# Optimization experiments

Measured on AMD Instinct MI355X. Metric: run time of the kernel, lower is better.

Reference implementation:

```python
import jax, jax.numpy as jnp
import numpy as np

N_HEADS = 16


def _apply_rope(x, rope):
    # x: [B, H, N, Dh], rope: [B, N, Dh]; consecutive (even, odd) pairs form complex numbers
    xr, xi = x[..., 0::2], x[..., 1::2]              # [B,H,N,Dh/2]
    rr, ri = rope[:, None, :, 0::2], rope[:, None, :, 1::2]  # [B,1,N,Dh/2]
    or_ = xr * rr - xi * ri
    oi = xr * ri + xi * rr
    return jnp.stack([or_, oi], axis=-1).reshape(x.shape)


def setup_inputs() -> dict:
    key = jax.random.key(0)
    ks = jax.random.split(key, 8)
    B, N, D, Dh = 2, 2048, 2048, 128
    s = 0.02
    return {
        "x": jax.random.normal(ks[0], (B, N, D), jnp.float32),
        "q_rope": jax.random.normal(ks[1], (B, N, Dh), jnp.float32),
        "k_rope": jax.random.normal(ks[2], (B, N, Dh), jnp.float32),
        "Wq": jax.random.normal(ks[3], (D, D), jnp.float32) * s,
        "Wk": jax.random.normal(ks[4], (D, D), jnp.float32) * s,
        "Wv": jax.random.normal(ks[5], (D, D), jnp.float32) * s,
        "Wo": jax.random.normal(ks[6], (D, D), jnp.float32) * s,
        "bo": jax.random.normal(ks[7], (D,), jnp.float32) * s,
    }


def reference(x, q_rope, k_rope, Wq, Wk, Wv, Wo, bo):
    B, N, D = x.shape
    H = N_HEADS
    Dh = D // H
    # QKV projections (weights stored as [in, out])
    q = (x @ Wq).reshape(B, N, H, Dh).transpose(0, 2, 1, 3)  # [B,H,N,Dh]
    k = (x @ Wk).reshape(B, N, H, Dh).transpose(0, 2, 1, 3)
    v = (x @ Wv).reshape(B, N, H, Dh).transpose(0, 2, 1, 3)
    # NOTE: original scales q by d_head^-0.5 AND F.sdpa applies its default
    # 1/sqrt(d_head) scale again -> total score scale 1/d_head (faithful).
    q = q * (Dh ** -0.5)
    q = _apply_rope(q, q_rope)
    k = _apply_rope(k, k_rope)
    scores = jnp.einsum('bhnd,bhmd->bhnm', q, k) * (Dh ** -0.5)
    attn = jax.nn.softmax(scores, axis=-1)
    out = jnp.einsum('bhnm,bhmd->bhnd', attn, v)  # [B,H,N,Dh]
    out = out.transpose(0, 2, 1, 3).reshape(B, N, D)
    return out @ Wo + bo
```

## Files before the change

kernel.cpp:

```cpp
#include <hip/hip_runtime.h>
#include <hip/hip_bf16.h>
#include <stdint.h>


typedef __attribute__((ext_vector_type(4))) float f32x4;
typedef __attribute__((ext_vector_type(8))) short bf16x8;

__device__ __forceinline__ unsigned short f2bf(float f){
  unsigned u = __builtin_bit_cast(unsigned, f);
  u += 0x7FFFu + ((u >> 16) & 1u);
  return (unsigned short)(u >> 16);
}
__device__ __forceinline__ float bf2f(unsigned short h){
  unsigned u = ((unsigned)h) << 16;
  return __builtin_bit_cast(float, u);
}
__device__ __forceinline__ void gload16(const void* g, void* l){
  __builtin_amdgcn_global_load_lds((const __attribute__((address_space(1))) void*)g,
                                   (__attribute__((address_space(3))) void*)l, 16, 0, 0);
}
__device__ __forceinline__ void drain_all(){
  asm volatile("s_waitcnt vmcnt(0) lgkmcnt(0)" ::: "memory");
  __builtin_amdgcn_sched_barrier(0);
}

__global__ void k_prep(const float* __restrict__ W0, const float* __restrict__ W1,
                       const float* __restrict__ W2, const float* __restrict__ W3,
                       unsigned short* __restrict__ WT,
                       const float* __restrict__ x, unsigned short* __restrict__ xb){
  if (blockIdx.z == 4){
    int bid = blockIdx.y * 32 + blockIdx.x;
    int t = threadIdx.x;
    #pragma unroll
    for (int it = 0; it < 8; it++){
      int i = bid * 2048 + it * 256 + t;
      float4 v = ((const float4*)x)[i];
      unsigned long long pk = (unsigned long long)f2bf(v.x)
        | ((unsigned long long)f2bf(v.y) << 16)
        | ((unsigned long long)f2bf(v.z) << 32)
        | ((unsigned long long)f2bf(v.w) << 48);
      ((unsigned long long*)xb)[i] = pk;
    }
    return;
  }
  const float* W = (blockIdx.z == 0) ? W0 : (blockIdx.z == 1) ? W1 : (blockIdx.z == 2) ? W2 : W3;
  unsigned short* dst = WT + (size_t)blockIdx.z * 4194304;
  __shared__ float tile[64][65];
  int t = threadIdx.x;
  int cc = t & 63, rb = t >> 6;
  int bx = blockIdx.x * 64;
  int by = blockIdx.y * 64;
  #pragma unroll
  for (int i = 0; i < 16; i++){
    int r = rb + i * 4;
    tile[r][cc] = W[(size_t)(by + r) * 2048 + bx + cc];
  }
  __syncthreads();
  #pragma unroll
  for (int i = 0; i < 16; i++){
    int r = rb + i * 4;
    dst[(size_t)(bx + r) * 2048 + by + cc] = f2bf(tile[cc][r]);
  }
}

__global__ __launch_bounds__(256, 4) void k_gemm_qkv(
    const unsigned short* __restrict__ A,
    const unsigned short* __restrict__ Bt,
    unsigned short* __restrict__ Oq,
    unsigned short* __restrict__ Ok,
    unsigned short* __restrict__ Ov,
    const float* __restrict__ ropeq,
    const float* __restrict__ ropek)
{
  const int Kdim = 2048;
  __shared__ unsigned short As[128 * 64];
  __shared__ unsigned short Bs[128 * 64];
  const int tid = threadIdx.x;
  const int w = tid >> 6, l = tid & 63, g = l >> 4, c = l & 15;
  const int i0 = blockIdx.y * 32 + blockIdx.x;
  const int xcd = i0 & 7, r0 = i0 >> 3;
  const int bm = (xcd * 4 + (r0 & 3)) * 128;
  const int bn = (r0 >> 2) * 128;
  const int mw = (w >> 1) * 64, nw = (w & 1) * 64;
  f32x4 acc[4][4] = {};
  const int srow = l >> 3;
  const int sbyte = (((l & 7) ^ srow) << 4);
  const char* Ab = (const char*)A;
  const char* Bb = (const char*)Bt;
  char* AsB = (char*)As; char* BsB = (char*)Bs;

  for (int kt = 0; kt < Kdim; kt += 64){
    __syncthreads();
    #pragma unroll
    for (int j = 0; j < 4; j++){
      int chunk = w * 4 + j;
      int row = chunk * 8 + srow;
      gload16(Ab + ((size_t)(bm + row) * Kdim + kt) * 2 + sbyte, AsB + chunk * 1024);
      gload16(Bb + ((size_t)(bn + row) * Kdim + kt) * 2 + sbyte, BsB + chunk * 1024);
    }
    __syncthreads();
    #pragma unroll
    for (int kk = 0; kk < 2; kk++){
      bf16x8 av[4], bv[4];
      #pragma unroll
      for (int i = 0; i < 4; i++){
        int m = mw + i * 16 + c;
        av[i] = *(const bf16x8*)(AsB + m * 128 + ((kk * 64 + g * 16) ^ ((m & 7) << 4)));
        int n = nw + i * 16 + c;
        bv[i] = *(const bf16x8*)(BsB + n * 128 + ((kk * 64 + g * 16) ^ ((n & 7) << 4)));
      }
      #pragma unroll
      for (int i = 0; i < 4; i++)
        #pragma unroll
        for (int jj = 0; jj < 4; jj++)
          acc[i][jj] = __builtin_amdgcn_mfma_f32_16x16x32_bf16(av[i], bv[jj], acc[i][jj], 0, 0, 0);
    }
  }

  const int matsel = bn >> 11;
  const int hh = (bn >> 7) & 15;
  if (matsel < 2){
    unsigned short* O = matsel ? Ok : Oq;
    const float* rope = matsel ? ropek : ropeq;
    const float scale = matsel ? 1.0f : (1.44269504088896f / 128.0f);
    #pragma unroll
    for (int i = 0; i < 4; i++){
      int m0 = bm + mw + i * 16 + g * 4;
      #pragma unroll
      for (int jj = 0; jj < 4; jj++){
        int d = nw + jj * 16 + c;
        int dbase = d & ~1;
        int odd = d & 1;
        #pragma unroll
        for (int r = 0; r < 4; r++){
          int m = m0 + r;
          int b = m >> 11, tok = m & 2047;
          float v = acc[i][jj][r];
          float vp = __shfl_xor(v, 1);
          float2 rv = *(const float2*)(rope + (((size_t)(b * 2048 + tok)) << 7) + dbase);
          float xr = odd ? vp : v;
          float xi = odd ? v : vp;
          float res = odd ? (xr * rv.y + xi * rv.x) : (xr * rv.x - xi * rv.y);
          O[(((size_t)(b * 16 + hh) * 2048 + tok) << 7) + d] = f2bf(res * scale);
        }
      }
    }
  } else {
    #pragma unroll
    for (int i = 0; i < 4; i++){
      int m0 = bm + mw + i * 16 + g * 4;
      int b = m0 >> 11, tok0 = m0 & 2047;
      #pragma unroll
      for (int jj = 0; jj < 4; jj++){
        int d = nw + jj * 16 + c;
        unsigned long long pk = (unsigned long long)f2bf(acc[i][jj][0])
          | ((unsigned long long)f2bf(acc[i][jj][1]) << 16)
          | ((unsigned long long)f2bf(acc[i][jj][2]) << 32)
          | ((unsigned long long)f2bf(acc[i][jj][3]) << 48);
        *(unsigned long long*)(Ov + ((size_t)(b * 16 + hh) * 128 + d) * 2048 + tok0) = pk;
      }
    }
  }
}

__global__ __launch_bounds__(512, 2) void k_gemm_out(
    const unsigned short* __restrict__ A,
    const unsigned short* __restrict__ Bt,
    float* __restrict__ O,
    const float* __restrict__ bias)
{
  const int Kdim = 2048;
  __shared__ char sh[98304];
  const int tid = threadIdx.x;
  const int w = tid >> 6, l = tid & 63, g = l >> 4, c = l & 15;
  const int i0 = blockIdx.y * 16 + blockIdx.x;
  const int xcd = i0 & 7, r0 = i0 >> 3;
  const int bm = (xcd * 2 + (r0 & 1)) * 256;
  const int bn = (r0 >> 1) * 128;
  const int mw = (w >> 1) * 64, nw = (w & 1) * 64;
  f32x4 acc[4][4] = {};
  const int srow = l >> 3;
  const int sbyte = (((l & 7) ^ srow) << 4);
  const char* Ab = (const char*)A;
  const char* Bb = (const char*)Bt;

  auto stage = [&](int kt, int buf){
    char* Abuf = sh + buf * 49152;
    char* Bbuf = Abuf + 32768;
    #pragma unroll
    for (int j = 0; j < 4; j++){
      int ch = w * 4 + j;
      int row = ch * 8 + srow;
      gload16(Ab + ((size_t)(bm + row) * Kdim + kt) * 2 + sbyte, Abuf + ch * 1024);
    }
    #pragma unroll
    for (int j = 0; j < 2; j++){
      int ch = w * 2 + j;
      int row = ch * 8 + srow;
      gload16(Bb + ((size_t)(bn + row) * Kdim + kt) * 2 + sbyte, Bbuf + ch * 1024);
    }
  };

  stage(0, 0);
  drain_all();
  __syncthreads();
  for (int t = 0; t < 32; t++){
    int cur = t & 1;
    if (t < 31) stage((t + 1) * 64, cur ^ 1);
    char* Abuf = sh + cur * 49152;
    char* Bbuf = Abuf + 32768;
    #pragma unroll
    for (int kk = 0; kk < 2; kk++){
      bf16x8 av[4], bv[4];
      #pragma unroll
      for (int i = 0; i < 4; i++){
        int m = mw + i * 16 + c;
        av[i] = *(const bf16x8*)(Abuf + m * 128 + ((kk * 64 + g * 16) ^ ((m & 7) << 4)));
        int n = nw + i * 16 + c;
        bv[i] = *(const bf16x8*)(Bbuf + n * 128 + ((kk * 64 + g * 16) ^ ((n & 7) << 4)));
      }
      #pragma unroll
      for (int i = 0; i < 4; i++)
        #pragma unroll
        for (int jj = 0; jj < 4; jj++)
          acc[i][jj] = __builtin_amdgcn_mfma_f32_16x16x32_bf16(av[i], bv[jj], acc[i][jj], 0, 0, 0);
    }
    drain_all();
    __syncthreads();
  }
  #pragma unroll
  for (int i = 0; i < 4; i++){
    int m0 = bm + mw + i * 16 + g * 4;
    #pragma unroll
    for (int jj = 0; jj < 4; jj++){
      int n = bn + nw + jj * 16 + c;
      float bv2 = bias[n];
      #pragma unroll
      for (int r = 0; r < 4; r++)
        O[(size_t)(m0 + r) * 2048 + n] = acc[i][jj][r] + bv2;
    }
  }
}

__global__ __launch_bounds__(256, 2) void k_attn(
    const unsigned short* __restrict__ Q,
    const unsigned short* __restrict__ Kg,
    const unsigned short* __restrict__ VT,
    unsigned short* __restrict__ Ao)
{
  __shared__ char sh[81920];
  char* PsB = sh + 65536;
  const int tid = threadIdx.x;
  const int w = tid >> 6, l = tid & 63, g = l >> 4, c = l & 15;
  const int i0 = blockIdx.y * 16 + blockIdx.x;
  const int xcd = i0 & 7, kb2 = i0 >> 3;
  const int bh = xcd * 4 + (kb2 >> 4);
  const int qt = kb2 & 15;
  const char* Qb = (const char*)(Q + (((size_t)bh * 2048 + qt * 128) << 7));
  const char* Kb = (const char*)(Kg + ((size_t)bh << 18));
  const char* Vb = (const char*)(VT + ((size_t)bh << 18));
  const int rsub = l >> 4;
  const int byte0 = (l & 15) << 4;
  const int drow = l >> 3;
  const int vbyte = (((l & 7) ^ drow) << 4);

  #pragma unroll
  for (int j = 0; j < 8; j++){
    int chunk = w * 8 + j;
    int row = chunk * 4 + rsub;
    gload16(Qb + (size_t)row * 256 + (byte0 ^ ((row & 7) << 4)), sh + chunk * 1024);
  }
  __syncthreads();
  bf16x8 qa[4][2];
  #pragma unroll
  for (int kk = 0; kk < 4; kk++)
    #pragma unroll
    for (int mf = 0; mf < 2; mf++){
      int q = w * 32 + mf * 16 + c;
      qa[kk][mf] = *(const bf16x8*)(sh + q * 256 + ((kk * 64 + g * 16) ^ ((q & 7) << 4)));
    }
  __syncthreads();

  auto stageKV = [&](int kv, int buf){
    char* Kc = sh + buf * 16384;
    char* Vc = sh + 32768 + buf * 16384;
    #pragma unroll
    for (int j = 0; j < 4; j++){
      int chunk = w * 4 + j;
      int row = chunk * 4 + rsub;
      gload16(Kb + (size_t)(kv * 64 + row) * 256 + (byte0 ^ ((row & 7) << 4)), Kc + chunk * 1024);
    }
    #pragma unroll
    for (int j = 0; j < 4; j++){
      int chunk = w * 4 + j;
      int d = chunk * 8 + drow;
      gload16(Vb + (size_t)d * 4096 + kv * 128 + vbyte, Vc + chunk * 1024);
    }
  };

  f32x4 oacc[2][8] = {};
  float lpart[2][4] = {};

  stageKV(0, 0);
  __syncthreads();

  for (int kv = 0; kv < 32; kv++){
    int cur = kv & 1;
    if (kv < 31) stageKV(kv + 1, cur ^ 1);
    char* Kc = sh + cur * 16384;
    char* Vc = sh + 32768 + cur * 16384;

    f32x4 sacc[2][4] = {};
    __builtin_amdgcn_s_setprio(1);
    #pragma unroll
    for (int kk = 0; kk < 4; kk++){
      bf16x8 kbf[4];
      #pragma unroll
      for (int nf = 0; nf < 4; nf++){
        int kx = nf * 16 + c;
        kbf[nf] = *(const bf16x8*)(Kc + kx * 256 + ((kk * 64 + g * 16) ^ ((kx & 7) << 4)));
      }
      #pragma unroll
      for (int mf = 0; mf < 2; mf++)
        #pragma unroll
        for (int nf = 0; nf < 4; nf++)
          sacc[mf][nf] = __builtin_amdgcn_mfma_f32_16x16x32_bf16(qa[kk][mf], kbf[nf], sacc[mf][nf], 0, 0, 0);
    }
    __builtin_amdgcn_s_setprio(0);

    #pragma unroll
    for (int mf = 0; mf < 2; mf++)
      #pragma unroll
      for (int nf = 0; nf < 4; nf++)
        #pragma unroll
        for (int r = 0; r < 4; r++){
          float pv = exp2f(sacc[mf][nf][r]);
          sacc[mf][nf][r] = pv;
          lpart[mf][r] += pv;
        }

    #pragma unroll
    for (int mf = 0; mf < 2; mf++)
      #pragma unroll
      for (int nf = 0; nf < 4; nf++)
        #pragma unroll
        for (int r = 0; r < 4; r++){
          int q = w * 32 + mf * 16 + g * 4 + r;
          int key = nf * 16 + c;
          *(unsigned short*)(PsB + q * 128 + ((key * 2) ^ (((q >> 2) & 3) << 5))) = f2bf(sacc[mf][nf][r]);
        }
    asm volatile("s_waitcnt lgkmcnt(0)" ::: "memory");
    __builtin_amdgcn_sched_barrier(0);

    __builtin_amdgcn_s_setprio(1);
    #pragma unroll
    for (int kk = 0; kk < 2; kk++){
      bf16x8 pa[2], vv[8];
      #pragma unroll
      for (int mf = 0; mf < 2; mf++){
        int q = w * 32 + mf * 16 + c;
        pa[mf] = *(const bf16x8*)(PsB + q * 128 + ((kk * 64 + g * 16) ^ (((q >> 2) & 3) << 5)));
      }
      #pragma unroll
      for (int df = 0; df < 8; df++){
        int d = df * 16 + c;
        vv[df] = *(const bf16x8*)(Vc + d * 128 + ((kk * 64 + g * 16) ^ ((d & 7) << 4)));
      }
      #pragma unroll
      for (int mf = 0; mf < 2; mf++)
        #pragma unroll
        for (int df = 0; df < 8; df++)
          oacc[mf][df] = __builtin_amdgcn_mfma_f32_16x16x32_bf16(pa[mf], vv[df], oacc[mf][df], 0, 0, 0);
    }
    __builtin_amdgcn_s_setprio(0);
    __syncthreads();
  }

  int b = bh >> 4, h = bh & 15;
  #pragma unroll
  for (int mf = 0; mf < 2; mf++)
    #pragma unroll
    for (int r = 0; r < 4; r++){
      float s = lpart[mf][r];
      #pragma unroll
      for (int off = 1; off < 16; off <<= 1) s += __shfl_xor(s, off);
      float inv = 1.f / s;
      int qg = qt * 128 + w * 32 + mf * 16 + g * 4 + r;
      size_t rowbase = ((size_t)(b * 2048 + qg)) * 2048 + h * 128;
      #pragma unroll
      for (int df = 0; df < 8; df++)
        Ao[rowbase + df * 16 + c] = f2bf(oacc[mf][df][r] * inv);
    }
}

extern "C" void kernel_launch(void* const* d_in, const int* in_sizes, int n_in,
                              void* d_out, int out_size, void* d_ws, size_t ws_size,
                              hipStream_t stream){
  const float* x      = (const float*)d_in[0];
  const float* q_rope = (const float*)d_in[1];
  const float* k_rope = (const float*)d_in[2];
  const float* Wq     = (const float*)d_in[3];
  const float* Wk     = (const float*)d_in[4];
  const float* Wv     = (const float*)d_in[5];
  const float* Wo     = (const float*)d_in[6];
  const float* bo     = (const float*)d_in[7];
  char* ws = (char*)d_ws;
  unsigned short* xb  = (unsigned short*)(ws);
  unsigned short* wqT = (unsigned short*)(ws + 16777216);
  unsigned short* woT = (unsigned short*)(ws + 41943040);
  unsigned short* qb  = (unsigned short*)(ws + 50331648);
  unsigned short* kbf = (unsigned short*)(ws + 67108864);
  unsigned short* vt  = (unsigned short*)(ws + 83886080);
  unsigned short* ab  = (unsigned short*)(ws + 100663296);

  dim3 tg(32, 32, 5);
  k_prep<<<tg, 256, 0, stream>>>(Wq, Wk, Wv, Wo, wqT, x, xb);
  dim3 gq(32, 48);
  k_gemm_qkv<<<gq, 256, 0, stream>>>(xb, wqT, qb, kbf, vt, q_rope, k_rope);
  dim3 ga(16, 32);
  k_attn<<<ga, 256, 0, stream>>>(qb, kbf, vt, ab);
  dim3 go(16, 16);
  k_gemm_out<<<go, 512, 0, stream>>>(ab, woT, (float*)d_out, bo);
}
```

Measured before the change: 276.7 us.

## Double-buffer LDS tiles in QKV GEMM with async prefetch two steps ahead

The QKV projection GEMM now uses two LDS buffers of 32KB each and issues global-to-LDS loads for tile t+2 while computing tile t, waiting with vmcnt(8) instead of a full drain. This is meant to overlap global memory latency with MFMA work. It doubles LDS usage to 64KB, so launch bounds drop from 4 to 2 blocks per CU, which reduces occupancy.

```diff
diff --git a/kernel.cpp b/kernel.cpp
--- a/kernel.cpp
+++ b/kernel.cpp
@@ -63,7 +63,7 @@
   }
 }
 
-__global__ __launch_bounds__(256, 4) void k_gemm_qkv(
+__global__ __launch_bounds__(256, 2) void k_gemm_qkv(
     const unsigned short* __restrict__ A,
     const unsigned short* __restrict__ Bt,
     unsigned short* __restrict__ Oq,
@@ -73,8 +73,7 @@
     const float* __restrict__ ropek)
 {
   const int Kdim = 2048;
-  __shared__ unsigned short As[128 * 64];
-  __shared__ unsigned short Bs[128 * 64];
+  __shared__ char sh[65536];
   const int tid = threadIdx.x;
   const int w = tid >> 6, l = tid & 63, g = l >> 4, c = l & 15;
   const int i0 = blockIdx.y * 32 + blockIdx.x;
@@ -87,18 +86,31 @@
   const int sbyte = (((l & 7) ^ srow) << 4);
   const char* Ab = (const char*)A;
   const char* Bb = (const char*)Bt;
-  char* AsB = (char*)As; char* BsB = (char*)Bs;
-
-  for (int kt = 0; kt < Kdim; kt += 64){
-    __syncthreads();
+
+  auto stage = [&](int tstep, int buf){
+    int kt = tstep * 64;
+    char* Abuf = sh + buf * 32768;
+    char* Bbuf = Abuf + 16384;
     #pragma unroll
     for (int j = 0; j < 4; j++){
       int chunk = w * 4 + j;
       int row = chunk * 8 + srow;
-      gload16(Ab + ((size_t)(bm + row) * Kdim + kt) * 2 + sbyte, AsB + chunk * 1024);
-      gload16(Bb + ((size_t)(bn + row) * Kdim + kt) * 2 + sbyte, BsB + chunk * 1024);
-    }
-    __syncthreads();
+      gload16(Ab + ((size_t)(bm + row) * Kdim + kt) * 2 + sbyte, Abuf + chunk * 1024);
+      gload16(Bb + ((size_t)(bn + row) * Kdim + kt) * 2 + sbyte, Bbuf + chunk * 1024);
+    }
+  };
+
+  stage(0, 0);
+  stage(1, 1);
+  for (int t = 0; t < 32; t++){
+    int cur = t & 1;
+    if (t < 31) asm volatile("s_waitcnt vmcnt(8)" ::: "memory");
+    else        asm volatile("s_waitcnt vmcnt(0)" ::: "memory");
+    __builtin_amdgcn_sched_barrier(0);
+    __builtin_amdgcn_s_barrier();
+    __builtin_amdgcn_sched_barrier(0);
+    char* AsB = sh + cur * 32768;
+    char* BsB = AsB + 16384;
     #pragma unroll
     for (int kk = 0; kk < 2; kk++){
       bf16x8 av[4], bv[4];
@@ -115,6 +127,9 @@
         for (int jj = 0; jj < 4; jj++)
           acc[i][jj] = __builtin_amdgcn_mfma_f32_16x16x32_bf16(av[i], bv[jj], acc[i][jj], 0, 0, 0);
     }
+    __builtin_amdgcn_s_barrier();
+    __builtin_amdgcn_sched_barrier(0);
+    if (t + 2 < 32) stage(t + 2, cur);
   }
 
   const int matsel = bn >> 11;
```

Result: faster. 266.8 us (-3.6%).
